# Kernel tuning notes

Hardware: AMD Instinct MI355X
Metric: run time of the kernel (lower is better)

The kernel has to match this reference:

```python
import jax, jax.numpy as jnp
import numpy as np

VERY_SMOL_NUM = -1e9  # undefined global in source; interpreted as large negative mask value
D_K = 128


def setup_inputs() -> dict:
    key = jax.random.key(0)
    k1, k2, k3 = jax.random.split(key, 3)
    B, S, D = 16, 2048, D_K
    Q = jax.random.normal(k1, (B, S, D), dtype=jnp.float32)
    K = jax.random.normal(k2, (B, S, D), dtype=jnp.float32)
    V = jax.random.normal(k3, (B, S, D), dtype=jnp.float32)
    return {"Q": Q, "K": K, "V": V}


def reference(Q, K, V):
    B, S, d_k = Q.shape
    # scores: [B, S, S] = Q @ K^T, scaled by 1/sqrt(d_k)
    x = jnp.einsum("bqd,bkd->bqk", Q, K) / jnp.sqrt(jnp.asarray(d_k, Q.dtype))
    # mask() is called unconditionally in the source (masked=False -> applied once):
    # add strict upper-triangular VERY_SMOL_NUM
    tri = jnp.triu(jnp.ones((S, S), dtype=x.dtype), k=1) * jnp.asarray(VERY_SMOL_NUM, x.dtype)
    x = x + tri  # broadcasts over batch, matching torch.triu on full shape
    # Softmax over dim=1 (query axis), as in the source (torch.nn.Softmax(dim=1))
    x = jax.nn.softmax(x, axis=1)
    return jnp.einsum("bqk,bkd->bqd", x, V)
```

## Files before the change

### kernel.cpp

```cpp
#include <hip/hip_runtime.h>


#define B_ 16
#define S_ 2048
#define D_ 128
#define QSCALE 0.12751744416825963f
#define NEG_BIG -1e30f
#define NCH 16
#define CHQ 128
#define PB 2162688

#define ROWW 136

#define LDS_BARRIER()                                  \
  do {                                                 \
    asm volatile("s_waitcnt lgkmcnt(0)" ::: "memory"); \
    __builtin_amdgcn_s_barrier();                      \
    __builtin_amdgcn_sched_barrier(0);                 \
  } while (0)

typedef short bf16x8 __attribute__((ext_vector_type(8)));
typedef float f32x4 __attribute__((ext_vector_type(4)));
typedef unsigned short u16x4 __attribute__((ext_vector_type(4)));
typedef unsigned int u32x2 __attribute__((ext_vector_type(2)));

#if defined(__has_builtin)
#if __has_builtin(__builtin_amdgcn_exp2f)
#define EXP2F(x) __builtin_amdgcn_exp2f(x)
#endif
#endif
#ifndef EXP2F
extern "C" __device__ float __ocml_exp2_f32(float);
#define EXP2F(x) __ocml_exp2_f32(x)
#endif

static __device__ __forceinline__ unsigned short f2bf(float f) {
  unsigned int u = __builtin_bit_cast(unsigned int, f);
  u += 0x7FFFu + ((u >> 16) & 1u);
  return (unsigned short)(u >> 16);
}

__global__ __launch_bounds__(256) void sdpa_convert(
    const float* __restrict__ Qr, const float* __restrict__ Kr,
    unsigned short* __restrict__ Qb, unsigned short* __restrict__ Kb) {
  const size_t t = (size_t)blockIdx.x * 256 + threadIdx.x;
  const float* src = blockIdx.y ? Kr : Qr;
  unsigned short* dstp = blockIdx.y ? Kb : Qb;
  const float sc = blockIdx.y ? 1.0f : QSCALE;
  f32x4 x = ((const f32x4*)src)[t];
  u16x4 o;
#pragma unroll
  for (int j = 0; j < 4; ++j) o[j] = f2bf(x[j] * sc);
  ((u16x4*)dstp)[t] = o;
}

__global__ __launch_bounds__(256, 4) void sdpa_pass1(
    const short* __restrict__ Qb, const short* __restrict__ Kb,
    float* __restrict__ lp_ws, unsigned short* __restrict__ Pt) {
  const int bid = blockIdx.x;
  int j = bid >> 4;
  int g = 0;
  while (j >= NCH - g) {
    j -= NCH - g;
    ++g;
  }
  const int ci = g + j;
  const int b = (bid & 7) + 8 * ((bid >> 3) & 1);

  __shared__ __align__(16) short Qst[2][32 * ROWW];
  const int tid = threadIdx.x;
  const int w = tid >> 6, lane = tid & 63, quad = lane >> 4, l15 = lane & 15;
  const int gg = 2 * g + (w >> 1);
  const int gb = 64 * gg;
  const int kb = gb + (w & 1) * 32;

  const size_t koff = ((size_t)b * S_ + kb + l15) * D_ + quad * 8;
  bf16x8 kh0[4], kh1[4];
#pragma unroll
  for (int c = 0; c < 4; ++c) {
    kh0[c] = *(const bf16x8*)(Kb + koff + c * 32);
    kh1[c] = *(const bf16x8*)(Kb + koff + 16 * D_ + c * 32);
  }

  const int nrp = S_ - gb;
  const size_t grp =
      (size_t)4 * ((size_t)gg * S_ - (size_t)(32 * gg) * (gg - 1));
  unsigned short* pw0 = Pt + (size_t)b * PB +
                        16 * (grp + (size_t)(2 * (w & 1)) * nrp) + quad * 4;
  unsigned short* pw1 = pw0 + (size_t)16 * nrp;

  const int sr = tid >> 3, sseg = tid & 7;
  const int q_start = CHQ * ci;

  {
    const short* sq = Qb + ((size_t)(b * S_ + q_start + sr)) * D_ + sseg * 16;
    bf16x8 h0 = *(const bf16x8*)(sq), h1 = *(const bf16x8*)(sq + 8);
    short* dst = &Qst[0][sr * ROWW + sseg * 16];
    *(bf16x8*)(dst) = h0;
    *(bf16x8*)(dst + 8) = h1;
  }
  LDS_BARRIER();

#define EMIT(q0s_, ktb_, cA_, pw_, lp_)                                       \
  do {                                                                        \
    float s0_ = cA_[0], s1_ = cA_[1], s2_ = cA_[2], s3_ = cA_[3];             \
    if ((q0s_) < (ktb_) + 16) {              \
      const int q_ = (q0s_) + l15;                                            \
      if ((ktb_) + quad * 4 + 0 > q_) s0_ = NEG_BIG;                          \
      if ((ktb_) + quad * 4 + 1 > q_) s1_ = NEG_BIG;                          \
      if ((ktb_) + quad * 4 + 2 > q_) s2_ = NEG_BIG;                          \
      if ((ktb_) + quad * 4 + 3 > q_) s3_ = NEG_BIG;                          \
    }                                                                         \
    const float e0_ = EXP2F(s0_), e1_ = EXP2F(s1_);                           \
    const float e2_ = EXP2F(s2_), e3_ = EXP2F(s3_);                           \
    lp_[0] += e0_;                                                            \
    lp_[1] += e1_;                                                            \
    lp_[2] += e2_;                                                            \
    lp_[3] += e3_;                                                            \
    unsigned int w0_, w1_;                                                    \
    asm("v_cvt_pk_bf16_f32 %0, %1, %2" : "=v"(w0_) : "v"(e0_), "v"(e1_));     \
    asm("v_cvt_pk_bf16_f32 %0, %1, %2" : "=v"(w1_) : "v"(e2_), "v"(e3_));     \
    u32x2 pk2_ = {w0_, w1_};                                                  \
    __builtin_nontemporal_store(                                              \
        pk2_, (u32x2*)((pw_) + (size_t)((q0s_)-gb + l15) * 16));              \
  } while (0)

  f32x4 lp0 = {0.f, 0.f, 0.f, 0.f}, lp1 = {0.f, 0.f, 0.f, 0.f};
#pragma unroll
  for (int it = 0; it < 4; ++it) {
    const int q0 = q_start + it * 32;
    const int cur = it & 1;
    bf16x8 h0, h1;
    if (it < 3) {
      const short* sq =
          Qb + ((size_t)(b * S_ + q0 + 32 + sr)) * D_ + sseg * 16;
      h0 = *(const bf16x8*)(sq);
      h1 = *(const bf16x8*)(sq + 8);
    }
#pragma unroll
    for (int sub = 0; sub < 2; ++sub) {
      const int q0s = q0 + sub * 16;
      if (q0s >= gb) {
        const short* rowp = &Qst[cur][(sub * 16 + l15) * ROWW + quad * 8];
        bf16x8 q0v = *(const bf16x8*)(rowp);
        bf16x8 q1v = *(const bf16x8*)(rowp + 32);
        bf16x8 q2v = *(const bf16x8*)(rowp + 64);
        bf16x8 q3v = *(const bf16x8*)(rowp + 96);
        f32x4 c0 = {0.f, 0.f, 0.f, 0.f};
        f32x4 c1 = {0.f, 0.f, 0.f, 0.f};
        c0 = __builtin_amdgcn_mfma_f32_16x16x32_bf16(kh0[0], q0v, c0, 0, 0, 0);
        c1 = __builtin_amdgcn_mfma_f32_16x16x32_bf16(kh1[0], q0v, c1, 0, 0, 0);
        c0 = __builtin_amdgcn_mfma_f32_16x16x32_bf16(kh0[1], q1v, c0, 0, 0, 0);
        c1 = __builtin_amdgcn_mfma_f32_16x16x32_bf16(kh1[1], q1v, c1, 0, 0, 0);
        c0 = __builtin_amdgcn_mfma_f32_16x16x32_bf16(kh0[2], q2v, c0, 0, 0, 0);
        c1 = __builtin_amdgcn_mfma_f32_16x16x32_bf16(kh1[2], q2v, c1, 0, 0, 0);
        c0 = __builtin_amdgcn_mfma_f32_16x16x32_bf16(kh0[3], q3v, c0, 0, 0, 0);
        c1 = __builtin_amdgcn_mfma_f32_16x16x32_bf16(kh1[3], q3v, c1, 0, 0, 0);
        EMIT(q0s, kb, c0, pw0, lp0);
        EMIT(q0s, kb + 16, c1, pw1, lp1);
      }
    }
    if (it < 3) {
      short* dst = &Qst[1 - cur][sr * ROWW + sseg * 16];
      *(bf16x8*)(dst) = h0;
      *(bf16x8*)(dst + 8) = h1;
    }
    LDS_BARRIER();
  }
#undef EMIT

#pragma unroll
  for (int d = 1; d < 16; d <<= 1) {
#pragma unroll
    for (int r = 0; r < 4; ++r) {
      lp0[r] += __shfl_xor(lp0[r], d, 64);
      lp1[r] += __shfl_xor(lp1[r], d, 64);
    }
  }
  if (l15 == 0) {
    float* dst = lp_ws + ((size_t)b * NCH + ci) * S_ + kb;
    *(f32x4*)(dst + quad * 4) = lp0;
    *(f32x4*)(dst + 16 + quad * 4) = lp1;
  }
}

__global__ __launch_bounds__(256) void sdpa_vscale(
    const float* __restrict__ Vr, const float* __restrict__ lp_ws,
    unsigned short* __restrict__ Vf) {
  __shared__ float Vld[32][132];
  __shared__ float as[32];
  const int kt = blockIdx.x, b = blockIdx.y, tid = threadIdx.x;
  const int k0 = kt * 32;
  const int row = tid >> 3, seg = tid & 7;
  const float* src = Vr + ((size_t)(b * S_ + k0 + row)) * D_ + seg * 16;
#pragma unroll
  for (int j = 0; j < 4; ++j) {
    f32x4 x = *(const f32x4*)(src + 4 * j);
    *(f32x4*)&Vld[row][seg * 16 + 4 * j] = x;
  }
  if (tid < 32) {
    const int k = k0 + tid;
    const int first = k >> 7;
    float l = 0.f;
#pragma unroll
    for (int ci = 0; ci < NCH; ++ci)
      if (ci >= first) l += lp_ws[((size_t)b * NCH + ci) * S_ + k];
    as[tid] = 1.0f / l;
  }
  __syncthreads();
  unsigned short* dst = Vf + ((size_t)(b * 64 + kt)) * 4096 + (size_t)tid * 16;
#pragma unroll
  for (int i = 0; i < 2; ++i) {
    const int u = tid * 2 + i;
    const int dt = u >> 6, l15 = (u >> 2) & 15, quad = u & 3;
    bf16x8 o;
#pragma unroll
    for (int e = 0; e < 8; ++e) {
      const int k = quad * 8 + e;
      o[e] = (short)f2bf(Vld[k][dt * 16 + l15] * as[k]);
    }
    *(bf16x8*)(dst + i * 8) = o;
  }
}

__global__ __launch_bounds__(256, 3) void sdpa_pass2(
    const unsigned short* __restrict__ Pt,
    const unsigned short* __restrict__ Vf, float* __restrict__ Out) {
  const int bid = blockIdx.x;
  const int b = (bid & 7) + 8 * ((bid >> 3) & 1);
  const int jj = bid >> 4;
  const int dh = jj & 1;
  const int py = jj >> 1;
  const int tid = threadIdx.x;
  const int w = tid >> 6, lane = tid & 63, quad = lane >> 4, l15 = lane & 15;

  const unsigned short* Pb = Pt + (size_t)b * PB + (quad & 1) * 8;
  const unsigned short* Vbase = Vf + (size_t)b * 64 * 4096 +
                                (size_t)(dh * 4) * 512 + l15 * 32 + quad * 8;
  const int qsel = quad >> 1;

#define LOADT(tp_, A0_, A1_, V_)                                             \
  do {                                                                       \
    const int nr_ = S_ - 64 * (tp_);                                         \
    const int pitch_ = 16 * nr_;                                             \
    const unsigned short* p0_ =                                              \
        Pb + 2048 * (tp_) * (65 - (tp_)) + qsel * pitch_ +                   \
        (qwl - 64 * (tp_)) * 16;                                             \
    A0_ = __builtin_nontemporal_load((const bf16x8*)p0_);                    \
    A1_ = __builtin_nontemporal_load((const bf16x8*)(p0_ + 2 * pitch_));     \
    const unsigned short* v0_ = Vbase + (size_t)(2 * (tp_)) * 4096;          \
    _Pragma("unroll") for (int d_ = 0; d_ < 4; ++d_) {                       \
      V_[d_] = *(const bf16x8*)(v0_ + d_ * 512);                             \
      V_[d_ + 4] = *(const bf16x8*)(v0_ + 4096 + d_ * 512);                  \
    }                                                                        \
  } while (0)

#define MMAT(A0_, A1_, V_)                                                   \
  do {                                                                       \
    _Pragma("unroll") for (int d_ = 0; d_ < 4; ++d_) acc[d_] =               \
        __builtin_amdgcn_mfma_f32_16x16x32_bf16(A0_, V_[d_], acc[d_], 0, 0,  \
                                                0);                          \
    _Pragma("unroll") for (int d_ = 0; d_ < 4; ++d_) acc[d_] =               \
        __builtin_amdgcn_mfma_f32_16x16x32_bf16(A1_, V_[d_ + 4], acc[d_], 0, \
                                                0, 0);                       \
  } while (0)

#pragma unroll
  for (int ti = 0; ti < 2; ++ti) {
    const int bx = ti ? (31 - py) : py;
    const int qw = 64 * bx + 16 * w;
    const int qwl = qw + l15;
    const int count = bx + 1;

    f32x4 acc[4];
#pragma unroll
    for (int d = 0; d < 4; ++d) acc[d] = (f32x4){0.f, 0.f, 0.f, 0.f};

    bf16x8 xA0, xA1, xV[8], yA0, yA1, yV[8];
    LOADT(0, xA0, xA1, xV);
    if (count > 1) LOADT(1, yA0, yA1, yV);
    int t = 0;
    for (; t + 2 <= count; t += 2) {
      MMAT(xA0, xA1, xV);
      if (t + 2 < count) LOADT(t + 2, xA0, xA1, xV);
      MMAT(yA0, yA1, yV);
      if (t + 3 < count) LOADT(t + 3, yA0, yA1, yV);
    }
    if (t < count) MMAT(xA0, xA1, xV);

#pragma unroll
    for (int r = 0; r < 4; ++r) {
      float* op =
          Out + ((size_t)b * S_ + qw + quad * 4 + r) * D_ + dh * 64 + l15;
#pragma unroll
      for (int d = 0; d < 4; ++d) op[d * 16] = acc[d][r];
    }
  }
#undef LOADT
#undef MMAT
}

extern "C" void kernel_launch(void* const* d_in, const int* in_sizes, int n_in,
                              void* d_out, int out_size, void* d_ws,
                              size_t ws_size, hipStream_t stream) {
  char* wsp = (char*)d_ws;
  float* lp_ws = (float*)wsp;
  char* p = wsp + (2 << 20);
  const size_t TSZ = (size_t)B_ * S_ * D_ * 2;
  unsigned short* Qb = (unsigned short*)(p);
  unsigned short* Kb = (unsigned short*)(p + TSZ);
  unsigned short* Vf = (unsigned short*)(p + 2 * TSZ);
  unsigned short* Pt = (unsigned short*)(p + 3 * TSZ);

  sdpa_convert<<<dim3((B_ * S_ * D_ / 4) / 256, 2), 256, 0, stream>>>(
      (const float*)d_in[0], (const float*)d_in[1], Qb, Kb);
  sdpa_pass1<<<dim3(NCH * 136), 256, 0, stream>>>(
      (const short*)Qb, (const short*)Kb, lp_ws, Pt);
  sdpa_vscale<<<dim3(S_ / 32, B_), 256, 0, stream>>>((const float*)d_in[2],
                                                     lp_ws, Vf);
  sdpa_pass2<<<dim3(512), 256, 0, stream>>>(Pt, Vf, (float*)d_out);
}
```

Measured before the change: 166.4 us.

## Share P tiles across both D halves via double-buffered LDS in pass2

```diff
diff --git a/kernel.cpp b/kernel.cpp
--- a/kernel.cpp
+++ b/kernel.cpp
@@ -11,12 +11,12 @@
 #define PB 2162688
 
 #define ROWW 136
+#define P2RW 24
 
 #define LDS_BARRIER()                                  \
   do {                                                 \
     asm volatile("s_waitcnt lgkmcnt(0)" ::: "memory"); \
     __builtin_amdgcn_s_barrier();                      \
-    __builtin_amdgcn_sched_barrier(0);                 \
   } while (0)
 
 typedef short bf16x8 __attribute__((ext_vector_type(8)));
@@ -121,8 +121,7 @@
     asm("v_cvt_pk_bf16_f32 %0, %1, %2" : "=v"(w0_) : "v"(e0_), "v"(e1_));     \
     asm("v_cvt_pk_bf16_f32 %0, %1, %2" : "=v"(w1_) : "v"(e2_), "v"(e3_));     \
     u32x2 pk2_ = {w0_, w1_};                                                  \
-    __builtin_nontemporal_store(                                              \
-        pk2_, (u32x2*)((pw_) + (size_t)((q0s_)-gb + l15) * 16));              \
+    *(u32x2*)((pw_) + (size_t)((q0s_)-gb + l15) * 16) = pk2_;                 \
   } while (0)
 
   f32x4 lp0 = {0.f, 0.f, 0.f, 0.f}, lp1 = {0.f, 0.f, 0.f, 0.f};
@@ -223,36 +222,41 @@
   }
 }
 
-__global__ __launch_bounds__(256, 3) void sdpa_pass2(
+__global__ __launch_bounds__(512, 2) void sdpa_pass2(
     const unsigned short* __restrict__ Pt,
     const unsigned short* __restrict__ Vf, float* __restrict__ Out) {
+  __shared__ __align__(16) short Pst[2][4 * 64 * P2RW];
   const int bid = blockIdx.x;
   const int b = (bid & 7) + 8 * ((bid >> 3) & 1);
-  const int jj = bid >> 4;
-  const int dh = jj & 1;
-  const int py = jj >> 1;
+  const int py = bid >> 4;
   const int tid = threadIdx.x;
   const int w = tid >> 6, lane = tid & 63, quad = lane >> 4, l15 = lane & 15;
-
-  const unsigned short* Pb = Pt + (size_t)b * PB + (quad & 1) * 8;
-  const unsigned short* Vbase = Vf + (size_t)b * 64 * 4096 +
+  const int qh = w & 3;
+  const int dh = w >> 2;
+
+  const int sp = tid >> 7, su = tid & 127, srow = su >> 1, sh = su & 1;
+
+  const unsigned short* Vbase = Vf + (size_t)b * (64 * 4096) +
                                 (size_t)(dh * 4) * 512 + l15 * 32 + quad * 8;
-  const int qsel = quad >> 1;
-
-#define LOADT(tp_, A0_, A1_, V_)                                             \
-  do {                                                                       \
-    const int nr_ = S_ - 64 * (tp_);                                         \
-    const int pitch_ = 16 * nr_;                                             \
-    const unsigned short* p0_ =                                              \
-        Pb + 2048 * (tp_) * (65 - (tp_)) + qsel * pitch_ +                   \
-        (qwl - 64 * (tp_)) * 16;                                             \
-    A0_ = __builtin_nontemporal_load((const bf16x8*)p0_);                    \
-    A1_ = __builtin_nontemporal_load((const bf16x8*)(p0_ + 2 * pitch_));     \
-    const unsigned short* v0_ = Vbase + (size_t)(2 * (tp_)) * 4096;          \
-    _Pragma("unroll") for (int d_ = 0; d_ < 4; ++d_) {                       \
-      V_[d_] = *(const bf16x8*)(v0_ + d_ * 512);                             \
-      V_[d_ + 4] = *(const bf16x8*)(v0_ + 4096 + d_ * 512);                  \
-    }                                                                        \
+  const int ard = ((quad >> 1) * 64 + 16 * qh + l15) * P2RW + (quad & 1) * 8;
+  const int awr = (sp * 64 + srow) * P2RW + sh * 8;
+
+#define VLOAD(tp_, V_)                                              \
+  do {                                                              \
+    const unsigned short* v0_ = Vbase + (size_t)(2 * (tp_)) * 4096; \
+    _Pragma("unroll") for (int d_ = 0; d_ < 4; ++d_) {              \
+      V_[d_] = *(const bf16x8*)(v0_ + d_ * 512);                    \
+      V_[d_ + 4] = *(const bf16x8*)(v0_ + 4096 + d_ * 512);         \
+    }                                                               \
+  } while (0)
+
+#define PLOAD(bx_, tp_, R_)                                                \
+  do {                                                                     \
+    const int pitch_ = 16 * (S_ - 64 * (tp_));                             \
+    const unsigned short* g_ = Pt + (size_t)b * PB +                       \
+                               2048 * (tp_) * (65 - (tp_)) + sp * pitch_ + \
+                               (64 * ((bx_) - (tp_)) + srow) * 16 + sh * 8; \
+    R_ = *(const bf16x8*)g_;                                               \
   } while (0)
 
 #define MMAT(A0_, A1_, V_)                                                   \
@@ -268,26 +272,51 @@
 #pragma unroll
   for (int ti = 0; ti < 2; ++ti) {
     const int bx = ti ? (31 - py) : py;
-    const int qw = 64 * bx + 16 * w;
-    const int qwl = qw + l15;
     const int count = bx + 1;
-
     f32x4 acc[4];
 #pragma unroll
     for (int d = 0; d < 4; ++d) acc[d] = (f32x4){0.f, 0.f, 0.f, 0.f};
 
-    bf16x8 xA0, xA1, xV[8], yA0, yA1, yV[8];
-    LOADT(0, xA0, xA1, xV);
-    if (count > 1) LOADT(1, yA0, yA1, yV);
-    int t = 0;
-    for (; t + 2 <= count; t += 2) {
-      MMAT(xA0, xA1, xV);
-      if (t + 2 < count) LOADT(t + 2, xA0, xA1, xV);
-      MMAT(yA0, yA1, yV);
-      if (t + 3 < count) LOADT(t + 3, yA0, yA1, yV);
-    }
-    if (t < count) MMAT(xA0, xA1, xV);
-
+    bf16x8 vA[8], vB[8], sreg;
+    __builtin_amdgcn_s_barrier();
+    PLOAD(bx, 0, sreg);
+    VLOAD(0, vA);
+    *(bf16x8*)&Pst[0][awr] = sreg;
+    LDS_BARRIER();
+
+    int tp = 0;
+    while (tp + 2 <= count) {
+      VLOAD(tp + 1, vB);
+      PLOAD(bx, tp + 1, sreg);
+      {
+        bf16x8 A0 = *(const bf16x8*)&Pst[tp & 1][ard];
+        bf16x8 A1 = *(const bf16x8*)&Pst[tp & 1][ard + 2 * 64 * P2RW];
+        MMAT(A0, A1, vA);
+      }
+      *(bf16x8*)&Pst[(tp & 1) ^ 1][awr] = sreg;
+      LDS_BARRIER();
+      if (tp + 2 < count) {
+        VLOAD(tp + 2, vA);
+        PLOAD(bx, tp + 2, sreg);
+      }
+      {
+        bf16x8 A0 = *(const bf16x8*)&Pst[(tp & 1) ^ 1][ard];
+        bf16x8 A1 = *(const bf16x8*)&Pst[(tp & 1) ^ 1][ard + 2 * 64 * P2RW];
+        MMAT(A0, A1, vB);
+      }
+      if (tp + 2 < count) {
+        *(bf16x8*)&Pst[tp & 1][awr] = sreg;
+      }
+      LDS_BARRIER();
+      tp += 2;
+    }
+    if (tp < count) {
+      bf16x8 A0 = *(const bf16x8*)&Pst[tp & 1][ard];
+      bf16x8 A1 = *(const bf16x8*)&Pst[tp & 1][ard + 2 * 64 * P2RW];
+      MMAT(A0, A1, vA);
+    }
+
+    const int qw = 64 * bx + 16 * qh;
 #pragma unroll
     for (int r = 0; r < 4; ++r) {
       float* op =
@@ -296,7 +325,8 @@
       for (int d = 0; d < 4; ++d) op[d * 16] = acc[d][r];
     }
   }
-#undef LOADT
+#undef VLOAD
+#undef PLOAD
 #undef MMAT
 }
 
@@ -318,5 +348,5 @@
       (const short*)Qb, (const short*)Kb, lp_ws, Pt);
   sdpa_vscale<<<dim3(S_ / 32, B_), 256, 0, stream>>>((const float*)d_in[2],
                                                      lp_ws, Vf);
-  sdpa_pass2<<<dim3(512), 256, 0, stream>>>(Pt, Vf, (float*)d_out);
-}
+  sdpa_pass2<<<dim3(256), 512, 0, stream>>>(Pt, Vf, (float*)d_out);
+}
```

New measurement: 158.4 us. 1.05x faster.
